# Kernel tuning notes

Hardware: AMD Instinct MI355X
Metric: run time of the kernel (lower is better)

The kernel has to match this reference:

```python
import jax, jax.numpy as jnp
import numpy as np

B, N, D = 32, 128, 64
E = N * N
EPS = 1e-5


def _bn(x, gamma, beta):
    # torch BatchNorm1d on (B, C, D): normalize per-channel over (batch, last dim)
    mean = jnp.mean(x, axis=(0, 2), keepdims=True)
    var = jnp.var(x, axis=(0, 2), keepdims=True)
    return (x - mean) * jax.lax.rsqrt(var + EPS) * gamma[None, :, None] + beta[None, :, None]


def _gat_layer(x, edge, Wh, We, Wp, Wa, gv, bv, ge, be):
    b, n, d = x.shape
    res = x
    z_h = jnp.einsum('bnd,od->bno', x, Wh)   # fc_h (torch Linear: y = x W^T)
    z_e = jnp.einsum('bed,od->beo', edge, We)  # fc_e
    # incidence matmuls are pure gathers: edge e = i*n + j
    z_src = jnp.broadcast_to(z_h[:, None, :, :], (b, n, n, d)).reshape(b, n * n, d)  # start: edge (i,j) <- node j
    z_dst = jnp.broadcast_to(z_h[:, :, None, :], (b, n, n, d)).reshape(b, n * n, d)  # end:   edge (i,j) <- node i
    z = jnp.concatenate([z_src, z_dst, z_e], axis=-1)  # (b, E, 3d)
    z_e_new = jnp.einsum('bec,oc->beo', z, Wp)  # fc_proj
    attn = jnp.einsum('bec,c->be', z, Wa[0])    # attn_fc -> (b, E)
    attn = jnp.where(attn >= 0, attn, 0.01 * attn)  # LeakyReLU(0.01)
    attn = jax.nn.softmax(attn.reshape(b, n, n), axis=2).reshape(b, n * n)  # softmax over sources j
    # scatter via end^T: node i <- sum_j attn[i,j] * z_src[i*n+j]
    agg = (attn[:, :, None] * z_src).reshape(b, n, n, d).sum(axis=2)
    x_new = jax.nn.elu(res + _bn(agg, gv, bv))
    edge_new = jax.nn.elu(_bn(z_e_new, ge, be))
    return x_new, edge_new


def setup_inputs():
    key = jax.random.key(0)
    ks = jax.random.split(key, 10)
    scale = float(np.sqrt(2.0 / D))
    return {
        'x': jax.random.normal(ks[0], (B, N, D), jnp.float32),
        'edge': jax.random.normal(ks[1], (B, E, D), jnp.float32),
        'Wh1': jax.random.normal(ks[2], (D, D), jnp.float32) * scale,
        'We1': jax.random.normal(ks[3], (D, D), jnp.float32) * scale,
        'Wp1': jax.random.normal(ks[4], (D, 3 * D), jnp.float32) * scale,
        'Wa1': jax.random.normal(ks[5], (1, 3 * D), jnp.float32) * scale,
        'Wh2': jax.random.normal(ks[6], (D, D), jnp.float32) * scale,
        'We2': jax.random.normal(ks[7], (D, D), jnp.float32) * scale,
        'Wp2': jax.random.normal(ks[8], (D, 3 * D), jnp.float32) * scale,
        'Wa2': jax.random.normal(ks[9], (1, 3 * D), jnp.float32) * scale,
        'gv1': jnp.ones((N,), jnp.float32), 'bv1': jnp.zeros((N,), jnp.float32),
        'ge1': jnp.ones((E,), jnp.float32), 'be1': jnp.zeros((E,), jnp.float32),
        'gv2': jnp.ones((N,), jnp.float32), 'bv2': jnp.zeros((N,), jnp.float32),
        'ge2': jnp.ones((E,), jnp.float32), 'be2': jnp.zeros((E,), jnp.float32),
    }


def reference(x, edge, Wh1, We1, Wp1, Wa1, Wh2, We2, Wp2, Wa2,
              gv1, bv1, ge1, be1, gv2, bv2, ge2, be2):
    x, edge = _gat_layer(x, edge, Wh1, We1, Wp1, Wa1, gv1, bv1, ge1, be1)
    x, edge = _gat_layer(x, edge, Wh2, We2, Wp2, Wa2, gv2, bv2, ge2, be2)
    return x, edge
```

## Files before the change

kernel.cpp:

```cpp
#include <hip/hip_runtime.h>
#include <math.h>

#define BB 32
#define NN 128
#define DD 64
#define EE (NN*NN)
#define EPSI 1e-5f

typedef __attribute__((ext_vector_type(8))) short bf16x8;
typedef __attribute__((ext_vector_type(4))) short s16x4;
typedef __attribute__((ext_vector_type(4))) float f32x4;

#define LGKM0() do { asm volatile("s_waitcnt lgkmcnt(0)" ::: "memory"); \
                     __builtin_amdgcn_sched_barrier(0); } while (0)

__device__ __forceinline__ short f2bf(float f) {
    union { float f; unsigned u; } v; v.f = f;
    unsigned u = v.u;
    unsigned r = (u + 0x7FFFu + ((u >> 16) & 1u)) >> 16;
    return (short)r;
}
__device__ __forceinline__ float bf2f(short s) {
    union { unsigned u; float f; } v; v.u = ((unsigned)(unsigned short)s) << 16;
    return v.f;
}
__device__ __forceinline__ float dot4(float4 a, float4 b) {
    return a.x*b.x + a.y*b.y + a.z*b.z + a.w*b.w;
}
__device__ __forceinline__ float elu(float v) {
    return v > 0.f ? v : __expf(v) - 1.f;
}

__global__ void k_node(const float* __restrict__ x, const float* __restrict__ Wh,
                       const float* __restrict__ Wp, const float* __restrict__ We,
                       const float* __restrict__ Wa,
                       float* __restrict__ zh, float* __restrict__ PsT,
                       float* __restrict__ PdT, float* __restrict__ sO,
                       float* __restrict__ tO,
                       short* __restrict__ Mbf, float* __restrict__ wf32)
{
    const int row = blockIdx.x;
    const int d = threadIdx.x;
    if (row >= BB*NN) {
        const int ff = row - BB*NN;
        float acc = 0.f;
        for (int o = 0; o < DD; ++o)
            acc += Wp[ff*192 + 128 + o] * We[o*DD + d];
        Mbf[ff*DD + d] = f2bf(acc);
        if (ff == 0) {
            float aw = 0.f;
            for (int o = 0; o < DD; ++o)
                aw += Wa[128 + o] * We[o*DD + d];
            wf32[d] = aw;
        }
        return;
    }
    const int b = row >> 7, n = row & 127;
    __shared__ float xr[DD];
    __shared__ float zr[DD];
    xr[d] = x[row*DD + d];
    __syncthreads();
    float acc = 0.f;
#pragma unroll
    for (int k = 0; k < DD; ++k) acc += xr[k] * Wh[d*DD + k];
    zr[d] = acc;
    zh[row*DD + d] = acc;
    __syncthreads();
    float a0 = 0.f, a1 = 0.f;
#pragma unroll
    for (int o = 0; o < DD; ++o) {
        float z = zr[o];
        a0 += Wp[d*192 + o]      * z;
        a1 += Wp[d*192 + 64 + o] * z;
    }
    const int fi = ((b >> 4)*4 + (d >> 4))*256 + (((b >> 2) & 3)*16 + (d & 15))*4 + (b & 3);
    PsT[n*2048 + fi] = a0;
    PdT[n*2048 + fi] = a1;
    float sv = zr[d] * Wa[d];
    float tv = zr[d] * Wa[64 + d];
#pragma unroll
    for (int off = 32; off; off >>= 1) {
        sv += __shfl_xor(sv, off);
        tv += __shfl_xor(tv, off);
    }
    if (d == 0) { sO[row] = sv; tO[row] = tv; }
}

template <int INM, int OUTM>
__global__ __launch_bounds__(256, 3) void k_edge(
    const void* __restrict__ einv,
    const short* __restrict__ Mbf,
    const float* __restrict__ wf32,
    const float* __restrict__ PsT,
    const float* __restrict__ PdT,
    const float* __restrict__ ge, const float* __restrict__ be,
    void* __restrict__ eoutv, float* __restrict__ uout)
{
    __shared__ short As[8][32][72];
    const int t  = threadIdx.x;
    const int l  = t & 63;
    const int wv = t >> 6;
    const int lr = l & 15;
    const int lg = l >> 4;
    const int e0 = blockIdx.x * 8;
    const int i0 = e0 >> 7;

    if constexpr (INM == 0) {
        const float* ein = (const float*)einv;
        const int g  = t >> 4;
        const int d0 = (t & 15) * 4;
        const int el = g & 7;
        const int bb = g >> 3;
        const float4 wv4 = *reinterpret_cast<const float4*>(wf32 + d0);
        float4 sv[16];
#pragma unroll
        for (int it = 0; it < 16; ++it) {
            const int b = bb + 2*it;
            sv[it] = *reinterpret_cast<const float4*>(
                         ein + ((size_t)b*EE + e0 + el)*DD + d0);
        }
#pragma unroll
        for (int it = 0; it < 16; ++it) {
            const int b = bb + 2*it;
            s16x4 o;
            o[0] = f2bf(sv[it].x); o[1] = f2bf(sv[it].y);
            o[2] = f2bf(sv[it].z); o[3] = f2bf(sv[it].w);
            *reinterpret_cast<s16x4*>(&As[el][b][d0]) = o;
            float up = dot4(sv[it], wv4);
            up += __shfl_xor(up, 1);
            up += __shfl_xor(up, 2);
            up += __shfl_xor(up, 4);
            up += __shfl_xor(up, 8);
            if ((t & 15) == 0) uout[(size_t)b*EE + e0 + el] = up;
        }
        __syncthreads();
    }

    bf16x8 bfr[4][2];
#pragma unroll
    for (int n = 0; n < 4; ++n)
#pragma unroll
        for (int s = 0; s < 2; ++s)
            bfr[n][s] = *reinterpret_cast<const bf16x8*>(Mbf + (16*n + lr)*DD + s*32 + lg*8);

    float4 wlo[2], whi[2];
    if constexpr (INM == 1) {
#pragma unroll
        for (int s = 0; s < 2; ++s) {
            wlo[s] = *reinterpret_cast<const float4*>(wf32 + s*32 + lg*8);
            whi[s] = *reinterpret_cast<const float4*>(wf32 + s*32 + lg*8 + 4);
        }
    }

    f32x4 acc[2][2][4];
#pragma unroll
    for (int ch = 0; ch < 2; ++ch) {
        const int e  = e0 + 2*wv + ch;
        const int j0 = e & 127;
        const float* psb = PsT + j0*2048;
        const float* pdb = PdT + i0*2048;
#pragma unroll
        for (int m = 0; m < 2; ++m)
#pragma unroll
            for (int n = 0; n < 4; ++n) {
                const float4 a = *reinterpret_cast<const float4*>(psb + (m*4+n)*256 + l*4);
                const float4 c = *reinterpret_cast<const float4*>(pdb + (m*4+n)*256 + l*4);
                acc[ch][m][n] = (f32x4){a.x+c.x, a.y+c.y, a.z+c.z, a.w+c.w};
            }
    }

#pragma unroll
    for (int ch = 0; ch < 2; ++ch) {
        const int e = e0 + 2*wv + ch;
        bf16x8 afr[2][2];
        if constexpr (INM == 0) {
#pragma unroll
            for (int m = 0; m < 2; ++m)
#pragma unroll
                for (int s = 0; s < 2; ++s)
                    afr[m][s] = *reinterpret_cast<const bf16x8*>(
                                    &As[2*wv + ch][16*m + lr][s*32 + lg*8]);
        } else {
            const short* ein = (const short*)einv + (size_t)e*BB*DD;
#pragma unroll
            for (int m = 0; m < 2; ++m)
#pragma unroll
                for (int s = 0; s < 2; ++s)
                    afr[m][s] = *reinterpret_cast<const bf16x8*>(
                                    ein + (16*m + lr)*DD + s*32 + lg*8);
#pragma unroll
            for (int m = 0; m < 2; ++m) {
                float up = 0.f;
#pragma unroll
                for (int s = 0; s < 2; ++s) {
                    up += bf2f(afr[m][s][0])*wlo[s].x + bf2f(afr[m][s][1])*wlo[s].y
                        + bf2f(afr[m][s][2])*wlo[s].z + bf2f(afr[m][s][3])*wlo[s].w
                        + bf2f(afr[m][s][4])*whi[s].x + bf2f(afr[m][s][5])*whi[s].y
                        + bf2f(afr[m][s][6])*whi[s].z + bf2f(afr[m][s][7])*whi[s].w;
                }
                up += __shfl_xor(up, 16);
                up += __shfl_xor(up, 32);
                if (lg == 0) uout[(size_t)(16*m + lr)*EE + e] = up;
            }
        }
#pragma unroll
        for (int m = 0; m < 2; ++m) {
#pragma unroll
            for (int n = 0; n < 4; ++n)
                acc[ch][m][n] = __builtin_amdgcn_mfma_f32_16x16x32_bf16(afr[m][0], bfr[n][0], acc[ch][m][n], 0, 0, 0);
#pragma unroll
            for (int n = 0; n < 4; ++n)
                acc[ch][m][n] = __builtin_amdgcn_mfma_f32_16x16x32_bf16(afr[m][1], bfr[n][1], acc[ch][m][n], 0, 0, 0);
        }
    }

    float s1a = 0.f, s2a = 0.f, s1b = 0.f, s2b = 0.f;
#pragma unroll
    for (int m = 0; m < 2; ++m)
#pragma unroll
        for (int n = 0; n < 4; ++n)
#pragma unroll
            for (int q = 0; q < 4; ++q) {
                float va = acc[0][m][n][q]; s1a += va; s2a += va*va;
                float vb = acc[1][m][n][q]; s1b += vb; s2b += vb*vb;
            }
#pragma unroll
    for (int off = 1; off < 64; off <<= 1) {
        s1a += __shfl_xor(s1a, off);
        s2a += __shfl_xor(s2a, off);
        s1b += __shfl_xor(s1b, off);
        s2b += __shfl_xor(s2b, off);
    }
    float scs[2], shs[2];
    {
        const int eA = e0 + 2*wv;
        float mean = s1a * (1.f/2048.f);
        float var  = s2a * (1.f/2048.f) - mean*mean;
        scs[0] = ge[eA] * rsqrtf(var + EPSI);
        shs[0] = be[eA] - mean*scs[0];
        mean = s1b * (1.f/2048.f);
        var  = s2b * (1.f/2048.f) - mean*mean;
        scs[1] = ge[eA+1] * rsqrtf(var + EPSI);
        shs[1] = be[eA+1] - mean*scs[1];
    }

#pragma unroll
    for (int ch = 0; ch < 2; ++ch)
#pragma unroll
        for (int m = 0; m < 2; ++m)
#pragma unroll
            for (int n = 0; n < 4; ++n)
#pragma unroll
                for (int q = 0; q < 4; ++q)
                    acc[ch][m][n][q] = elu(acc[ch][m][n][q]*scs[ch] + shs[ch]);

    LGKM0();
#pragma unroll
    for (int ch = 0; ch < 2; ++ch) {
        const int e = e0 + 2*wv + ch;
        float (*Z)[68] = reinterpret_cast<float (*)[68]>(&As[2*wv + ch][0][0]);
#pragma unroll
        for (int h = 0; h < 2; ++h) {
#pragma unroll
            for (int n = 0; n < 4; ++n)
#pragma unroll
                for (int q = 0; q < 4; ++q)
                    Z[4*lg + q][16*n + lr] = acc[ch][h][n][q];
            LGKM0();
            if constexpr (OUTM == 0) {
                float* eout = (float*)eoutv;
#pragma unroll
                for (int it = 0; it < 4; ++it) {
                    const int rr = lg + 4*it;
                    const int b  = 16*h + rr;
                    float4 z = *reinterpret_cast<float4*>(&Z[rr][lr*4]);
                    *reinterpret_cast<float4*>(eout + ((size_t)b*EE + e)*DD + lr*4) = z;
                }
            } else {
                short* eout = (short*)eoutv + (size_t)e*BB*DD;
#pragma unroll
                for (int it = 0; it < 2; ++it) {
                    const int rr = (l >> 3) + 8*it;
                    const int b  = 16*h + rr;
                    const int c0 = (l & 7)*8;
                    float4 zlo = *reinterpret_cast<float4*>(&Z[rr][c0]);
                    float4 zhi = *reinterpret_cast<float4*>(&Z[rr][c0+4]);
                    bf16x8 o;
                    o[0]=f2bf(zlo.x); o[1]=f2bf(zlo.y); o[2]=f2bf(zlo.z); o[3]=f2bf(zlo.w);
                    o[4]=f2bf(zhi.x); o[5]=f2bf(zhi.y); o[6]=f2bf(zhi.z); o[7]=f2bf(zhi.w);
                    *reinterpret_cast<bf16x8*>(eout + b*DD + c0) = o;
                }
            }
            LGKM0();
        }
    }
}

__global__ void k_attn(const float* __restrict__ sI, const float* __restrict__ tI,
                       const float* __restrict__ u, const float* __restrict__ zh,
                       float* __restrict__ agg)
{
    int blk = blockIdx.x; int b = blk >> 7, i = blk & 127;
    int l = threadIdx.x;
    __shared__ float at[NN];
    float ti = tI[blk];
    float l0 = sI[b*NN + l]      + ti + u[b*EE + i*NN + l];
    float l1 = sI[b*NN + l + 64] + ti + u[b*EE + i*NN + l + 64];
    l0 = l0 >= 0.f ? l0 : 0.01f*l0;
    l1 = l1 >= 0.f ? l1 : 0.01f*l1;
    float mx = fmaxf(l0, l1);
#pragma unroll
    for (int off = 32; off; off >>= 1) mx = fmaxf(mx, __shfl_xor(mx, off));
    float e0 = __expf(l0 - mx), e1 = __expf(l1 - mx);
    float sm = e0 + e1;
#pragma unroll
    for (int off = 32; off; off >>= 1) sm += __shfl_xor(sm, off);
    float inv = 1.f / sm;
    at[l]      = e0 * inv;
    at[l + 64] = e1 * inv;
    __syncthreads();
    float acc = 0.f;
    for (int j = 0; j < NN; ++j) acc += at[j] * zh[(b*NN + j)*DD + l];
    agg[(b*NN + i)*DD + l] = acc;
}

__global__ void k_vbn(const float* __restrict__ agg, const float* __restrict__ xres,
                      const float* __restrict__ gv, const float* __restrict__ bv,
                      float* __restrict__ xout)
{
    int i = blockIdx.x, t = threadIdx.x;
    float vals[8];
    float s1 = 0.f, s2 = 0.f;
#pragma unroll
    for (int q = 0; q < 8; ++q) {
        int m = t + 256*q; int b = m >> 6, d = m & 63;
        float v = agg[(b*NN + i)*DD + d];
        vals[q] = v; s1 += v; s2 += v*v;
    }
#pragma unroll
    for (int off = 1; off < 64; off <<= 1) {
        s1 += __shfl_xor(s1, off);
        s2 += __shfl_xor(s2, off);
    }
    __shared__ float r1[4], r2[4];
    int wv = t >> 6;
    if ((t & 63) == 0) { r1[wv] = s1; r2[wv] = s2; }
    __syncthreads();
    s1 = r1[0] + r1[1] + r1[2] + r1[3];
    s2 = r2[0] + r2[1] + r2[2] + r2[3];
    float mean  = s1 * (1.f/2048.f);
    float var   = s2 * (1.f/2048.f) - mean*mean;
    float scale = gv[i] * rsqrtf(var + EPSI);
    float shift = bv[i] - mean*scale;
#pragma unroll
    for (int q = 0; q < 8; ++q) {
        int m = t + 256*q; int b = m >> 6, d = m & 63;
        float v = vals[q]*scale + shift + xres[(b*NN + i)*DD + d];
        xout[(b*NN + i)*DD + d] = v > 0.f ? v : __expf(v) - 1.f;
    }
}

extern "C" void kernel_launch(void* const* d_in, const int* in_sizes, int n_in,
                              void* d_out, int out_size, void* d_ws, size_t ws_size,
                              hipStream_t stream)
{
    const float* x    = (const float*)d_in[0];
    const float* edge = (const float*)d_in[1];
    const float* Wh1  = (const float*)d_in[2];
    const float* We1  = (const float*)d_in[3];
    const float* Wp1  = (const float*)d_in[4];
    const float* Wa1  = (const float*)d_in[5];
    const float* Wh2  = (const float*)d_in[6];
    const float* We2  = (const float*)d_in[7];
    const float* Wp2  = (const float*)d_in[8];
    const float* Wa2  = (const float*)d_in[9];
    const float* gv1  = (const float*)d_in[10];
    const float* bv1  = (const float*)d_in[11];
    const float* ge1  = (const float*)d_in[12];
    const float* be1  = (const float*)d_in[13];
    const float* gv2  = (const float*)d_in[14];
    const float* bv2  = (const float*)d_in[15];
    const float* ge2  = (const float*)d_in[16];
    const float* be2  = (const float*)d_in[17];

    float* xout = (float*)d_out;
    float* eout = (float*)d_out + BB*NN*DD;

    float* ws  = (float*)d_ws;
    short* Mbf = (short*)ws;  ws += DD*DD/2;
    float* wf  = ws;  ws += DD;
    float* zh  = ws;  ws += BB*NN*DD;
    float* PsT = ws;  ws += NN*BB*DD;
    float* PdT = ws;  ws += NN*BB*DD;
    float* sb  = ws;  ws += BB*NN;
    float* tb  = ws;  ws += BB*NN;
    float* ub  = ws;  ws += BB*EE;
    float* agg = ws;  ws += BB*NN*DD;
    float* x1  = ws;  ws += BB*NN*DD;
    short* e1bf = (short*)ws;
    const size_t need = ((size_t)(ws - (float*)d_ws))*4 + (size_t)EE*BB*DD*2;

    const bool dense = (ws_size >= need);

    k_node<<<BB*NN + 64, 64, 0, stream>>>(x, Wh1, Wp1, We1, Wa1, zh, PsT, PdT, sb, tb, Mbf, wf);
    if (dense)
        k_edge<0,1><<<EE/8, 256, 0, stream>>>(edge, Mbf, wf, PsT, PdT, ge1, be1, e1bf, ub);
    else
        k_edge<0,0><<<EE/8, 256, 0, stream>>>(edge, Mbf, wf, PsT, PdT, ge1, be1, eout, ub);
    k_attn<<<BB*NN, 64, 0, stream>>>(sb, tb, ub, zh, agg);
    k_vbn<<<NN, 256, 0, stream>>>(agg, x, gv1, bv1, x1);
    k_node<<<BB*NN + 64, 64, 0, stream>>>(x1, Wh2, Wp2, We2, Wa2, zh, PsT, PdT, sb, tb, Mbf, wf);
    if (dense)
        k_edge<1,0><<<EE/8, 256, 0, stream>>>(e1bf, Mbf, wf, PsT, PdT, ge2, be2, eout, ub);
    else
        k_edge<0,0><<<EE/8, 256, 0, stream>>>(eout, Mbf, wf, PsT, PdT, ge2, be2, eout, ub);
    k_attn<<<BB*NN, 64, 0, stream>>>(sb, tb, ub, zh, agg);
    k_vbn<<<NN, 256, 0, stream>>>(agg, x1, gv2, bv2, xout);
}
```

Measured before the change: 206.4 us.

## Stage fp32 edge tiles via async global-to-LDS loads, one edge per wave

The edge kernel now handles 4 edges per block (one per wave) instead of 8. The fp32 edge input is streamed straight into a swizzled LDS buffer with global_load_lds, instead of loading into registers, converting to bf16 and storing. The u-projection and the bf16 conversion now happen when the fragments are read from LDS. The fp32 output path also writes back through the swizzled LDS tile so global stores are coalesced, and launch bounds rise to 4 blocks per CU. The aim is to cut register pressure and load latency and raise occupancy, at the cost of twice as many blocks and more LDS traffic per edge.

```diff
diff --git a/kernel.cpp b/kernel.cpp
--- a/kernel.cpp
+++ b/kernel.cpp
@@ -8,10 +8,11 @@
 #define EPSI 1e-5f
 
 typedef __attribute__((ext_vector_type(8))) short bf16x8;
-typedef __attribute__((ext_vector_type(4))) short s16x4;
 typedef __attribute__((ext_vector_type(4))) float f32x4;
 
 #define LGKM0() do { asm volatile("s_waitcnt lgkmcnt(0)" ::: "memory"); \
+                     __builtin_amdgcn_sched_barrier(0); } while (0)
+#define VM0()   do { asm volatile("s_waitcnt vmcnt(0)" ::: "memory"); \
                      __builtin_amdgcn_sched_barrier(0); } while (0)
 
 __device__ __forceinline__ short f2bf(float f) {
@@ -23,9 +24,6 @@
 __device__ __forceinline__ float bf2f(short s) {
     union { unsigned u; float f; } v; v.u = ((unsigned)(unsigned short)s) << 16;
     return v.f;
-}
-__device__ __forceinline__ float dot4(float4 a, float4 b) {
-    return a.x*b.x + a.y*b.y + a.z*b.z + a.w*b.w;
 }
 __device__ __forceinline__ float elu(float v) {
     return v > 0.f ? v : __expf(v) - 1.f;
@@ -87,7 +85,7 @@
 }
 
 template <int INM, int OUTM>
-__global__ __launch_bounds__(256, 3) void k_edge(
+__global__ __launch_bounds__(256, 4) void k_edge(
     const void* __restrict__ einv,
     const short* __restrict__ Mbf,
     const float* __restrict__ wf32,
@@ -96,44 +94,27 @@
     const float* __restrict__ ge, const float* __restrict__ be,
     void* __restrict__ eoutv, float* __restrict__ uout)
 {
-    __shared__ short As[8][32][72];
+    __shared__ float SA[8704];
     const int t  = threadIdx.x;
     const int l  = t & 63;
     const int wv = t >> 6;
     const int lr = l & 15;
     const int lg = l >> 4;
-    const int e0 = blockIdx.x * 8;
+    const int e0 = blockIdx.x * 4;
+    const int e  = e0 + wv;
     const int i0 = e0 >> 7;
+    const int j0 = e & 127;
 
     if constexpr (INM == 0) {
         const float* ein = (const float*)einv;
-        const int g  = t >> 4;
-        const int d0 = (t & 15) * 4;
-        const int el = g & 7;
-        const int bb = g >> 3;
-        const float4 wv4 = *reinterpret_cast<const float4*>(wf32 + d0);
-        float4 sv[16];
-#pragma unroll
-        for (int it = 0; it < 16; ++it) {
-            const int b = bb + 2*it;
-            sv[it] = *reinterpret_cast<const float4*>(
-                         ein + ((size_t)b*EE + e0 + el)*DD + d0);
-        }
-#pragma unroll
-        for (int it = 0; it < 16; ++it) {
-            const int b = bb + 2*it;
-            s16x4 o;
-            o[0] = f2bf(sv[it].x); o[1] = f2bf(sv[it].y);
-            o[2] = f2bf(sv[it].z); o[3] = f2bf(sv[it].w);
-            *reinterpret_cast<s16x4*>(&As[el][b][d0]) = o;
-            float up = dot4(sv[it], wv4);
-            up += __shfl_xor(up, 1);
-            up += __shfl_xor(up, 2);
-            up += __shfl_xor(up, 4);
-            up += __shfl_xor(up, 8);
-            if ((t & 15) == 0) uout[(size_t)b*EE + e0 + el] = up;
-        }
-        __syncthreads();
+#pragma unroll
+        for (int r = 0; r < 8; ++r) {
+            const int b = 8*wv + r;
+            const float* gsrc = ein + ((size_t)b*EE + e0)*DD + ((l ^ (b & 7)) << 2);
+            __builtin_amdgcn_global_load_lds(
+                (const __attribute__((address_space(1))) unsigned*)gsrc,
+                (__attribute__((address_space(3))) unsigned*)&SA[b*256], 16, 0, 0);
+        }
     }
 
     bf16x8 bfr[4][2];
@@ -142,21 +123,15 @@
 #pragma unroll
         for (int s = 0; s < 2; ++s)
             bfr[n][s] = *reinterpret_cast<const bf16x8*>(Mbf + (16*n + lr)*DD + s*32 + lg*8);
-
     float4 wlo[2], whi[2];
-    if constexpr (INM == 1) {
-#pragma unroll
-        for (int s = 0; s < 2; ++s) {
-            wlo[s] = *reinterpret_cast<const float4*>(wf32 + s*32 + lg*8);
-            whi[s] = *reinterpret_cast<const float4*>(wf32 + s*32 + lg*8 + 4);
-        }
-    }
-
-    f32x4 acc[2][2][4];
-#pragma unroll
-    for (int ch = 0; ch < 2; ++ch) {
-        const int e  = e0 + 2*wv + ch;
-        const int j0 = e & 127;
+#pragma unroll
+    for (int s = 0; s < 2; ++s) {
+        wlo[s] = *reinterpret_cast<const float4*>(wf32 + s*32 + lg*8);
+        whi[s] = *reinterpret_cast<const float4*>(wf32 + s*32 + lg*8 + 4);
+    }
+
+    f32x4 acc[2][4];
+    {
         const float* psb = PsT + j0*2048;
         const float* pdb = PdT + i0*2048;
 #pragma unroll
@@ -165,133 +140,134 @@
             for (int n = 0; n < 4; ++n) {
                 const float4 a = *reinterpret_cast<const float4*>(psb + (m*4+n)*256 + l*4);
                 const float4 c = *reinterpret_cast<const float4*>(pdb + (m*4+n)*256 + l*4);
-                acc[ch][m][n] = (f32x4){a.x+c.x, a.y+c.y, a.z+c.z, a.w+c.w};
+                acc[m][n] = (f32x4){a.x+c.x, a.y+c.y, a.z+c.z, a.w+c.w};
             }
     }
 
-#pragma unroll
-    for (int ch = 0; ch < 2; ++ch) {
-        const int e = e0 + 2*wv + ch;
-        bf16x8 afr[2][2];
-        if constexpr (INM == 0) {
-#pragma unroll
-            for (int m = 0; m < 2; ++m)
-#pragma unroll
-                for (int s = 0; s < 2; ++s)
-                    afr[m][s] = *reinterpret_cast<const bf16x8*>(
-                                    &As[2*wv + ch][16*m + lr][s*32 + lg*8]);
-        } else {
-            const short* ein = (const short*)einv + (size_t)e*BB*DD;
-#pragma unroll
-            for (int m = 0; m < 2; ++m)
-#pragma unroll
-                for (int s = 0; s < 2; ++s)
-                    afr[m][s] = *reinterpret_cast<const bf16x8*>(
-                                    ein + (16*m + lr)*DD + s*32 + lg*8);
-#pragma unroll
-            for (int m = 0; m < 2; ++m) {
-                float up = 0.f;
-#pragma unroll
-                for (int s = 0; s < 2; ++s) {
-                    up += bf2f(afr[m][s][0])*wlo[s].x + bf2f(afr[m][s][1])*wlo[s].y
-                        + bf2f(afr[m][s][2])*wlo[s].z + bf2f(afr[m][s][3])*wlo[s].w
-                        + bf2f(afr[m][s][4])*whi[s].x + bf2f(afr[m][s][5])*whi[s].y
-                        + bf2f(afr[m][s][6])*whi[s].z + bf2f(afr[m][s][7])*whi[s].w;
+    bf16x8 afr[2][2];
+    if constexpr (INM == 0) {
+        VM0();
+        __syncthreads();
+#pragma unroll
+        for (int m = 0; m < 2; ++m) {
+            const int b = 16*m + lr;
+            float up = 0.f;
+#pragma unroll
+            for (int s = 0; s < 2; ++s) {
+                const int c = wv*16 + s*8 + lg*2;
+                const f32x4 lo = *reinterpret_cast<const f32x4*>(&SA[b*256 + (( c    ^ (b&7)) << 2)]);
+                const f32x4 hi = *reinterpret_cast<const f32x4*>(&SA[b*256 + (((c+1) ^ (b&7)) << 2)]);
+                up += lo[0]*wlo[s].x + lo[1]*wlo[s].y + lo[2]*wlo[s].z + lo[3]*wlo[s].w
+                    + hi[0]*whi[s].x + hi[1]*whi[s].y + hi[2]*whi[s].z + hi[3]*whi[s].w;
+                bf16x8 a;
+                a[0]=f2bf(lo[0]); a[1]=f2bf(lo[1]); a[2]=f2bf(lo[2]); a[3]=f2bf(lo[3]);
+                a[4]=f2bf(hi[0]); a[5]=f2bf(hi[1]); a[6]=f2bf(hi[2]); a[7]=f2bf(hi[3]);
+                afr[m][s] = a;
+            }
+            up += __shfl_xor(up, 16);
+            up += __shfl_xor(up, 32);
+            if (lg == 0) uout[(size_t)b*EE + e] = up;
+        }
+    } else {
+        const short* ein = (const short*)einv + (size_t)e*BB*DD;
+#pragma unroll
+        for (int m = 0; m < 2; ++m)
+#pragma unroll
+            for (int s = 0; s < 2; ++s)
+                afr[m][s] = *reinterpret_cast<const bf16x8*>(ein + (16*m + lr)*DD + s*32 + lg*8);
+#pragma unroll
+        for (int m = 0; m < 2; ++m) {
+            float up = 0.f;
+#pragma unroll
+            for (int s = 0; s < 2; ++s) {
+                up += bf2f(afr[m][s][0])*wlo[s].x + bf2f(afr[m][s][1])*wlo[s].y
+                    + bf2f(afr[m][s][2])*wlo[s].z + bf2f(afr[m][s][3])*wlo[s].w
+                    + bf2f(afr[m][s][4])*whi[s].x + bf2f(afr[m][s][5])*whi[s].y
+                    + bf2f(afr[m][s][6])*whi[s].z + bf2f(afr[m][s][7])*whi[s].w;
+            }
+            up += __shfl_xor(up, 16);
+            up += __shfl_xor(up, 32);
+            if (lg == 0) uout[(size_t)(16*m + lr)*EE + e] = up;
+        }
+    }
+
+#pragma unroll
+    for (int m = 0; m < 2; ++m) {
+#pragma unroll
+        for (int n = 0; n < 4; ++n)
+            acc[m][n] = __builtin_amdgcn_mfma_f32_16x16x32_bf16(afr[m][0], bfr[n][0], acc[m][n], 0, 0, 0);
+#pragma unroll
+        for (int n = 0; n < 4; ++n)
+            acc[m][n] = __builtin_amdgcn_mfma_f32_16x16x32_bf16(afr[m][1], bfr[n][1], acc[m][n], 0, 0, 0);
+    }
+
+    float s1 = 0.f, s2 = 0.f;
+#pragma unroll
+    for (int m = 0; m < 2; ++m)
+#pragma unroll
+        for (int n = 0; n < 4; ++n)
+#pragma unroll
+            for (int q = 0; q < 4; ++q) { float v = acc[m][n][q]; s1 += v; s2 += v*v; }
+#pragma unroll
+    for (int off = 1; off < 64; off <<= 1) {
+        s1 += __shfl_xor(s1, off);
+        s2 += __shfl_xor(s2, off);
+    }
+    const float mean = s1 * (1.f/2048.f);
+    const float var  = s2 * (1.f/2048.f) - mean*mean;
+    const float sc = ge[e] * rsqrtf(var + EPSI);
+    const float sh = be[e] - mean*sc;
+
+#pragma unroll
+    for (int m = 0; m < 2; ++m)
+#pragma unroll
+        for (int n = 0; n < 4; ++n)
+#pragma unroll
+            for (int q = 0; q < 4; ++q)
+                acc[m][n][q] = elu(acc[m][n][q]*sc + sh);
+
+    if constexpr (OUTM == 0) {
+        float* eout = (float*)eoutv;
+        __syncthreads();
+#pragma unroll
+        for (int m = 0; m < 2; ++m)
+#pragma unroll
+            for (int n = 0; n < 4; ++n)
+#pragma unroll
+                for (int q = 0; q < 4; ++q) {
+                    const int b = 16*m + 4*lg + q;
+                    const int c = wv*16 + 4*n + (lr >> 2);
+                    SA[b*256 + ((c ^ (b & 7)) << 2) + (lr & 3)] = acc[m][n][q];
                 }
-                up += __shfl_xor(up, 16);
-                up += __shfl_xor(up, 32);
-                if (lg == 0) uout[(size_t)(16*m + lr)*EE + e] = up;
-            }
-        }
-#pragma unroll
-        for (int m = 0; m < 2; ++m) {
+        __syncthreads();
+#pragma unroll
+        for (int r = 0; r < 8; ++r) {
+            const int b = 8*wv + r;
+            const f32x4 v = *reinterpret_cast<const f32x4*>(&SA[b*256 + ((l ^ (b & 7)) << 2)]);
+            *reinterpret_cast<f32x4*>(eout + ((size_t)b*EE + e0)*DD + 4*l) = v;
+        }
+    } else {
+        short* eoutp = (short*)eoutv + (size_t)e*BB*DD;
+        __syncthreads();
+        float (*Z)[68] = reinterpret_cast<float (*)[68]>(&SA[wv*2176]);
+#pragma unroll
+        for (int m = 0; m < 2; ++m)
 #pragma unroll
             for (int n = 0; n < 4; ++n)
-                acc[ch][m][n] = __builtin_amdgcn_mfma_f32_16x16x32_bf16(afr[m][0], bfr[n][0], acc[ch][m][n], 0, 0, 0);
-#pragma unroll
-            for (int n = 0; n < 4; ++n)
-                acc[ch][m][n] = __builtin_amdgcn_mfma_f32_16x16x32_bf16(afr[m][1], bfr[n][1], acc[ch][m][n], 0, 0, 0);
-        }
-    }
-
-    float s1a = 0.f, s2a = 0.f, s1b = 0.f, s2b = 0.f;
-#pragma unroll
-    for (int m = 0; m < 2; ++m)
-#pragma unroll
-        for (int n = 0; n < 4; ++n)
-#pragma unroll
-            for (int q = 0; q < 4; ++q) {
-                float va = acc[0][m][n][q]; s1a += va; s2a += va*va;
-                float vb = acc[1][m][n][q]; s1b += vb; s2b += vb*vb;
-            }
-#pragma unroll
-    for (int off = 1; off < 64; off <<= 1) {
-        s1a += __shfl_xor(s1a, off);
-        s2a += __shfl_xor(s2a, off);
-        s1b += __shfl_xor(s1b, off);
-        s2b += __shfl_xor(s2b, off);
-    }
-    float scs[2], shs[2];
-    {
-        const int eA = e0 + 2*wv;
-        float mean = s1a * (1.f/2048.f);
-        float var  = s2a * (1.f/2048.f) - mean*mean;
-        scs[0] = ge[eA] * rsqrtf(var + EPSI);
-        shs[0] = be[eA] - mean*scs[0];
-        mean = s1b * (1.f/2048.f);
-        var  = s2b * (1.f/2048.f) - mean*mean;
-        scs[1] = ge[eA+1] * rsqrtf(var + EPSI);
-        shs[1] = be[eA+1] - mean*scs[1];
-    }
-
-#pragma unroll
-    for (int ch = 0; ch < 2; ++ch)
-#pragma unroll
-        for (int m = 0; m < 2; ++m)
-#pragma unroll
-            for (int n = 0; n < 4; ++n)
 #pragma unroll
                 for (int q = 0; q < 4; ++q)
-                    acc[ch][m][n][q] = elu(acc[ch][m][n][q]*scs[ch] + shs[ch]);
-
-    LGKM0();
-#pragma unroll
-    for (int ch = 0; ch < 2; ++ch) {
-        const int e = e0 + 2*wv + ch;
-        float (*Z)[68] = reinterpret_cast<float (*)[68]>(&As[2*wv + ch][0][0]);
-#pragma unroll
-        for (int h = 0; h < 2; ++h) {
-#pragma unroll
-            for (int n = 0; n < 4; ++n)
-#pragma unroll
-                for (int q = 0; q < 4; ++q)
-                    Z[4*lg + q][16*n + lr] = acc[ch][h][n][q];
-            LGKM0();
-            if constexpr (OUTM == 0) {
-                float* eout = (float*)eoutv;
-#pragma unroll
-                for (int it = 0; it < 4; ++it) {
-                    const int rr = lg + 4*it;
-                    const int b  = 16*h + rr;
-                    float4 z = *reinterpret_cast<float4*>(&Z[rr][lr*4]);
-                    *reinterpret_cast<float4*>(eout + ((size_t)b*EE + e)*DD + lr*4) = z;
-                }
-            } else {
-                short* eout = (short*)eoutv + (size_t)e*BB*DD;
-#pragma unroll
-                for (int it = 0; it < 2; ++it) {
-                    const int rr = (l >> 3) + 8*it;
-                    const int b  = 16*h + rr;
-                    const int c0 = (l & 7)*8;
-                    float4 zlo = *reinterpret_cast<float4*>(&Z[rr][c0]);
-                    float4 zhi = *reinterpret_cast<float4*>(&Z[rr][c0+4]);
-                    bf16x8 o;
-                    o[0]=f2bf(zlo.x); o[1]=f2bf(zlo.y); o[2]=f2bf(zlo.z); o[3]=f2bf(zlo.w);
-                    o[4]=f2bf(zhi.x); o[5]=f2bf(zhi.y); o[6]=f2bf(zhi.z); o[7]=f2bf(zhi.w);
-                    *reinterpret_cast<bf16x8*>(eout + b*DD + c0) = o;
-                }
-            }
-            LGKM0();
+                    Z[16*m + 4*lg + q][16*n + lr] = acc[m][n][q];
+        LGKM0();
+#pragma unroll
+        for (int it = 0; it < 4; ++it) {
+            const int rr = (l >> 3) + 8*it;
+            const int c0 = (l & 7)*8;
+            const float4 zlo = *reinterpret_cast<const float4*>(&Z[rr][c0]);
+            const float4 zhi = *reinterpret_cast<const float4*>(&Z[rr][c0+4]);
+            bf16x8 o;
+            o[0]=f2bf(zlo.x); o[1]=f2bf(zlo.y); o[2]=f2bf(zlo.z); o[3]=f2bf(zlo.w);
+            o[4]=f2bf(zhi.x); o[5]=f2bf(zhi.y); o[6]=f2bf(zhi.z); o[7]=f2bf(zhi.w);
+            *reinterpret_cast<bf16x8*>(eoutp + rr*64 + c0) = o;
         }
     }
 }
@@ -404,16 +380,16 @@
 
     k_node<<<BB*NN + 64, 64, 0, stream>>>(x, Wh1, Wp1, We1, Wa1, zh, PsT, PdT, sb, tb, Mbf, wf);
     if (dense)
-        k_edge<0,1><<<EE/8, 256, 0, stream>>>(edge, Mbf, wf, PsT, PdT, ge1, be1, e1bf, ub);
+        k_edge<0,1><<<EE/4, 256, 0, stream>>>(edge, Mbf, wf, PsT, PdT, ge1, be1, e1bf, ub);
     else
-        k_edge<0,0><<<EE/8, 256, 0, stream>>>(edge, Mbf, wf, PsT, PdT, ge1, be1, eout, ub);
+        k_edge<0,0><<<EE/4, 256, 0, stream>>>(edge, Mbf, wf, PsT, PdT, ge1, be1, eout, ub);
     k_attn<<<BB*NN, 64, 0, stream>>>(sb, tb, ub, zh, agg);
     k_vbn<<<NN, 256, 0, stream>>>(agg, x, gv1, bv1, x1);
     k_node<<<BB*NN + 64, 64, 0, stream>>>(x1, Wh2, Wp2, We2, Wa2, zh, PsT, PdT, sb, tb, Mbf, wf);
     if (dense)
-        k_edge<1,0><<<EE/8, 256, 0, stream>>>(e1bf, Mbf, wf, PsT, PdT, ge2, be2, eout, ub);
+        k_edge<1,0><<<EE/4, 256, 0, stream>>>(e1bf, Mbf, wf, PsT, PdT, ge2, be2, eout, ub);
     else
-        k_edge<0,0><<<EE/8, 256, 0, stream>>>(eout, Mbf, wf, PsT, PdT, ge2, be2, eout, ub);
+        k_edge<0,0><<<EE/4, 256, 0, stream>>>(eout, Mbf, wf, PsT, PdT, ge2, be2, eout, ub);
     k_attn<<<BB*NN, 64, 0, stream>>>(sb, tb, ub, zh, agg);
     k_vbn<<<NN, 256, 0, stream>>>(agg, x1, gv2, bv2, xout);
 }
```

New measurement: 249.2 us. 1.21x slower.
